# Kernel tuning notes

Hardware: AMD Instinct MI355X
Metric: run time of the kernel (lower is better)

## Reference

```python
import jax, jax.numpy as jnp
import numpy as np

K = 3          # kernel size
STRIDE = 1
PAD = 1        # dilation*(K-1)//2
DIL = 1


def _bilinear_gather(x, py, px):
    """Bilinear sample x[B,C,H,W] at float coords (py,px) of shape [B,K2,Ho,Wo].
    Out-of-bounds contributions are zero (matches detectron2 DeformConv).
    Returns [B,C,K2,Ho,Wo]."""
    B, C, H, W = x.shape
    xf = x.reshape(B, C, H * W)
    y0 = jnp.floor(py)
    x0 = jnp.floor(px)
    out = jnp.zeros((B, C) + py.shape[1:], dtype=x.dtype)
    gather = jax.vmap(lambda xb, ib: xb[:, ib])  # ([C,HW],[K2,Ho,Wo])->[C,K2,Ho,Wo]
    for cy, cx in ((y0, x0), (y0, x0 + 1.0), (y0 + 1.0, x0), (y0 + 1.0, x0 + 1.0)):
        wgt = (1.0 - jnp.abs(py - cy)) * (1.0 - jnp.abs(px - cx))
        valid = (cy >= 0) & (cy <= H - 1) & (cx >= 0) & (cx <= W - 1)
        yi = jnp.clip(cy, 0, H - 1).astype(jnp.int32)
        xi = jnp.clip(cx, 0, W - 1).astype(jnp.int32)
        idx = yi * W + xi  # [B,K2,Ho,Wo]
        vals = gather(xf, idx)  # [B,C,K2,Ho,Wo]
        out = out + (wgt * valid.astype(x.dtype))[:, None] * vals
    return out


def _deform_conv(x, offset, weight):
    B, C, H, W = x.shape
    Ho = (H + 2 * PAD - (DIL * (K - 1) + 1)) // STRIDE + 1
    Wo = (W + 2 * PAD - (DIL * (K - 1) + 1)) // STRIDE + 1
    K2 = K * K
    # base sampling grid
    hs = (jnp.arange(Ho) * STRIDE - PAD).astype(x.dtype)  # [Ho]
    ws = (jnp.arange(Wo) * STRIDE - PAD).astype(x.dtype)  # [Wo]
    ky, kx = jnp.meshgrid(jnp.arange(K), jnp.arange(K), indexing='ij')
    ky = (ky.reshape(-1) * DIL).astype(x.dtype)  # [K2], row-major taps
    kx = (kx.reshape(-1) * DIL).astype(x.dtype)
    # offsets: channel 2k = dy, 2k+1 = dx for tap k
    off = offset.reshape(B, K2, 2, Ho, Wo)
    dy, dx = off[:, :, 0], off[:, :, 1]  # [B,K2,Ho,Wo]
    py = hs[None, None, :, None] + ky[None, :, None, None] + dy
    px = ws[None, None, None, :] + kx[None, :, None, None] + dx
    sampled = _bilinear_gather(x, py, px)  # [B,C,K2,Ho,Wo]
    wk = weight.reshape(weight.shape[0], C, K2)  # groups=1
    return jnp.einsum('ocK,bcKhw->bohw', wk, sampled)


def setup_inputs() -> dict:
    key = jax.random.key(0)
    k1, k2, k3 = jax.random.split(key, 3)
    B, C, H, W = 8, 256, 64, 64
    x = jax.random.normal(k1, (B, C, H, W), dtype=jnp.float32)
    offset = jax.random.normal(k2, (B, 2 * K * K, H, W), dtype=jnp.float32)
    weight = jax.random.normal(k3, (256, C, K, K), dtype=jnp.float32) * 0.02
    return {"x": x, "offset": offset, "weight": weight}


def reference(x, offset, weight):
    return _deform_conv(x, offset, weight)
```

## Files before the change

### kernel.cpp

```cpp
#include <hip/hip_runtime.h>
#include <stdint.h>


#define Bb 8
#define Cc 256
#define Hh 64
#define Ww 64
#define Pp 4096
#define Oo 256
#define NK2 9
#define NPAIR 36
#define BN 64
#define SROW 40
#define WT_BYTES (2u * 72u * 256u * 32u)

typedef __attribute__((ext_vector_type(4))) float f32x4;
typedef __attribute__((ext_vector_type(8))) short s16x8;
typedef __attribute__((ext_vector_type(4))) int   i32x4;

static __device__ __forceinline__ unsigned short f2bf(float f) {
    union { float f; uint32_t u; } v; v.f = f;
    return (unsigned short)((v.u + 0x7fffu + ((v.u >> 16) & 1u)) >> 16);
}
static __device__ __forceinline__ int imin(int a, int b) { return a < b ? a : b; }
static __device__ __forceinline__ int imax(int a, int b) { return a > b ? a : b; }

__global__ __launch_bounds__(256)
void prep(const float* __restrict__ x, const float* __restrict__ w,
          unsigned short* __restrict__ xt, unsigned short* __restrict__ wt) {
    __shared__ __align__(16) unsigned short L[9216];
    const int bx = blockIdx.x, tid = threadIdx.x;

    if (bx < 2048) {
        unsigned short (*t2)[72] = (unsigned short(*)[72])L;
        const int b = bx & 7, ti = bx >> 3;
        const int c0 = (ti & 3) * 64, p0 = (ti >> 2) * 64;
        #pragma unroll
        for (int rd = 0; rd < 4; rd++) {
            int c = (tid >> 4) + rd * 16;
            int px4 = (tid & 15) * 4;
            f32x4 fv = *(const f32x4*)&x[(size_t)(b * Cc + c0 + c) * Pp + p0 + px4];
            #pragma unroll
            for (int j = 0; j < 4; j++) {
                int px = px4 + j;
                int chunk = ((c >> 3) + px) & 7;
                t2[px][chunk * 8 + (c & 7)] = f2bf(fv[j]);
            }
        }
        __syncthreads();
        #pragma unroll
        for (int rd = 0; rd < 2; rd++) {
            int px = (tid >> 3) + rd * 32;
            int k = tid & 7;
            int chunk = (k + px) & 7;
            uint4 u = *(const uint4*)&t2[px][chunk * 8];
            *(uint4*)&xt[(size_t)(b * Pp + p0 + px) * Cc + c0 + k * 8] = u;
        }
    } else {
        const int o0 = (bx - 2048) * 4;
        #pragma unroll
        for (int r9 = 0; r9 < 9; r9++) {
            int idx = r9 * 256 + tid;
            f32x4 fv = *(const f32x4*)&w[(size_t)o0 * 2304 + (size_t)idx * 4];
            #pragma unroll
            for (int j = 0; j < 4; j++) L[idx * 4 + j] = f2bf(fv[j]);
        }
        __syncthreads();
        #pragma unroll 4
        for (int i = 0; i < 36; i++) {
            int ks = i * 2 + (tid >> 7);
            int r = (tid >> 5) & 3, c32 = tid & 31;
            int c = (ks & 7) * 32 + c32, k2 = ks >> 3;
            wt[(size_t)ks * 8192 + (o0 + r) * 32 + c32] = L[r * 2304 + c * 9 + k2];
        }
    }
}

__global__ __launch_bounds__(512, 4)
void dcn_main(const float* __restrict__ off, const unsigned short* __restrict__ wt,
              const unsigned short* __restrict__ xt, float* __restrict__ out) {
    __shared__ __align__(16) unsigned short Sl[2][2][BN][SROW];
    __shared__ __align__(16) int   tidx[NK2][BN][4];
    __shared__ __align__(16) float twgt[NK2][BN][4];

    const int b   = blockIdx.x & 7;
    const int p0  = (blockIdx.x >> 3) * BN;
    const int tid = threadIdx.x;
    const int lane = tid & 63;
    const int wv   = tid >> 6;
    const int quad = lane >> 4;
    const int l16  = lane & 15;
    const int moff = wv * 32;

    const int px  = tid >> 3;
    const int sub = tid & 7;
    const int hh_ = sub >> 2;
    const int cc_ = (sub & 3) * 8;

    const char* xtb = (const char*)xt + (size_t)b * Pp * Cc * 2;

    for (int t = tid; t < NK2 * BN; t += 512) {
        int k2 = t >> 6, pxl = t & 63;
        int pl = p0 + pxl;
        int hh = pl >> 6, ww = pl & 63;
        int ky = k2 / 3, kx = k2 - ky * 3;
        float dy = off[((size_t)(b * 18 + 2 * k2    ) * Pp) + pl];
        float dx = off[((size_t)(b * 18 + 2 * k2 + 1) * Pp) + pl];
        float py  = (float)(hh - 1 + ky) + dy;
        float pxf = (float)(ww - 1 + kx) + dx;
        float y0f = floorf(py), x0f = floorf(pxf);
        int   y0 = (int)y0f,  x0 = (int)x0f;
        int   y1 = y0 + 1,    x1 = x0 + 1;
        float ly = py - y0f,  lx = pxf - x0f;
        float oy = 1.f - ly,  ox = 1.f - lx;
        bool vy0 = (y0 >= 0) && (y0 < Hh);
        bool vy1 = (y1 >= 0) && (y1 < Hh);
        bool vx0 = (x0 >= 0) && (x0 < Ww);
        bool vx1 = (x1 >= 0) && (x1 < Ww);
        int cy0 = imin(imax(y0, 0), Hh - 1), cy1 = imin(imax(y1, 0), Hh - 1);
        int cx0 = imin(imax(x0, 0), Ww - 1), cx1 = imin(imax(x1, 0), Ww - 1);
        tidx[k2][pxl][0] = (cy0 * Ww + cx0) * 512;  twgt[k2][pxl][0] = (vy0 && vx0) ? oy * ox : 0.f;
        tidx[k2][pxl][1] = (cy0 * Ww + cx1) * 512;  twgt[k2][pxl][1] = (vy0 && vx1) ? oy * lx : 0.f;
        tidx[k2][pxl][2] = (cy1 * Ww + cx0) * 512;  twgt[k2][pxl][2] = (vy1 && vx0) ? ly * ox : 0.f;
        tidx[k2][pxl][3] = (cy1 * Ww + cx1) * 512;  twgt[k2][pxl][3] = (vy1 && vx1) ? ly * lx : 0.f;
    }
    __syncthreads();

    int   tio[4];
    float twv[4];
    uint4 g[4];
    {
        i32x4 ti = *(const i32x4*)&tidx[0][px][0];
        f32x4 tw = *(const f32x4*)&twgt[0][px][0];
        #pragma unroll
        for (int t = 0; t < 4; t++) { tio[t] = ti[t]; twv[t] = tw[t]; }
    }

    f32x4 acc[2][4];
    #pragma unroll
    for (int mt = 0; mt < 2; mt++)
        #pragma unroll
        for (int nt = 0; nt < 4; nt++) acc[mt][nt] = (f32x4){0.f, 0.f, 0.f, 0.f};

    auto reduce_store = [&](int prn) {
        float s0 = 0.f, s1 = 0.f, s2 = 0.f, s3 = 0.f, s4 = 0.f, s5 = 0.f, s6 = 0.f, s7 = 0.f;
        #pragma unroll
        for (int t = 0; t < 4; t++) {
            uint4 v = g[t];
            float wg = twv[t];
            s0 += wg * __uint_as_float(v.x << 16);
            s1 += wg * __uint_as_float(v.x);
            s2 += wg * __uint_as_float(v.y << 16);
            s3 += wg * __uint_as_float(v.y);
            s4 += wg * __uint_as_float(v.z << 16);
            s5 += wg * __uint_as_float(v.z);
            s6 += wg * __uint_as_float(v.w << 16);
            s7 += wg * __uint_as_float(v.w);
        }
        uint4 d;
        d.x = __builtin_amdgcn_perm(__float_as_uint(s1), __float_as_uint(s0), 0x07060302u);
        d.y = __builtin_amdgcn_perm(__float_as_uint(s3), __float_as_uint(s2), 0x07060302u);
        d.z = __builtin_amdgcn_perm(__float_as_uint(s5), __float_as_uint(s4), 0x07060302u);
        d.w = __builtin_amdgcn_perm(__float_as_uint(s7), __float_as_uint(s6), 0x07060302u);
        *(uint4*)&Sl[prn & 1][hh_][px][cc_] = d;
    };

    s16x8 afA[2][2], afB[2][2];

    auto step = [&](int pr, s16x8 (&cur)[2][2], s16x8 (&nxt)[2][2]) {
        __syncthreads();
        const int prn = pr + 1;
        if (prn < NPAIR) {
            if ((prn & 3) == 0) {
                int k2 = prn >> 2;
                i32x4 ti = *(const i32x4*)&tidx[k2][px][0];
                f32x4 tw = *(const f32x4*)&twgt[k2][px][0];
                #pragma unroll
                for (int t = 0; t < 4; t++) { tio[t] = ti[t]; twv[t] = tw[t]; }
            }
            const int coff = (prn & 3) * 128 + sub * 16;
            #pragma unroll
            for (int t = 0; t < 4; t++)
                g[t] = *(const uint4*)(xtb + tio[t] + coff);
            const char* wb = (const char*)wt + ((size_t)prn << 15);
            #pragma unroll
            for (int h = 0; h < 2; h++)
                #pragma unroll
                for (int mt = 0; mt < 2; mt++)
                    nxt[h][mt] = *(const s16x8*)(wb + h * 16384 +
                                                 (moff + mt * 16 + l16) * 64 + quad * 16);
        }
        s16x8 bfr[2][4];
        const char* sb = (const char*)&Sl[pr & 1][0][0][0];
        #pragma unroll
        for (int h = 0; h < 2; h++)
            #pragma unroll
            for (int nt = 0; nt < 4; nt++)
                bfr[h][nt] = *(const s16x8*)(sb + h * (BN * SROW * 2) +
                                             (nt * 16 + l16) * (SROW * 2) + quad * 16);
        #pragma unroll
        for (int h = 0; h < 2; h++)
            #pragma unroll
            for (int mt = 0; mt < 2; mt++)
                #pragma unroll
                for (int nt = 0; nt < 4; nt++)
                    acc[mt][nt] = __builtin_amdgcn_mfma_f32_16x16x32_bf16(
                        cur[h][mt], bfr[h][nt], acc[mt][nt], 0, 0, 0);
        if (prn < NPAIR) reduce_store(prn);
    };

    {
        #pragma unroll
        for (int t = 0; t < 4; t++)
            g[t] = *(const uint4*)(xtb + tio[t] + sub * 16);
        const char* wb = (const char*)wt;
        #pragma unroll
        for (int h = 0; h < 2; h++)
            #pragma unroll
            for (int mt = 0; mt < 2; mt++)
                afA[h][mt] = *(const s16x8*)(wb + h * 16384 +
                                             (moff + mt * 16 + l16) * 64 + quad * 16);
        reduce_store(0);
    }

    for (int pr = 0; pr < NPAIR; pr += 2) {
        step(pr,     afA, afB);
        step(pr + 1, afB, afA);
    }

    float* op = out + ((size_t)b * Oo) * Pp + p0;
    #pragma unroll
    for (int mt = 0; mt < 2; mt++)
        #pragma unroll
        for (int nt = 0; nt < 4; nt++)
            #pragma unroll
            for (int r = 0; r < 4; r++) {
                int o_ = moff + mt * 16 + quad * 4 + r;
                int p_ = nt * 16 + l16;
                op[(size_t)o_ * Pp + p_] = acc[mt][nt][r];
            }
}

extern "C" void kernel_launch(void* const* d_in, const int* in_sizes, int n_in,
                              void* d_out, int out_size, void* d_ws, size_t ws_size,
                              hipStream_t stream) {
    (void)in_sizes; (void)n_in; (void)out_size; (void)ws_size;
    const float* x   = (const float*)d_in[0];
    const float* off = (const float*)d_in[1];
    const float* w   = (const float*)d_in[2];
    float* out = (float*)d_out;

    unsigned short* wt = (unsigned short*)d_ws;
    unsigned short* xt = (unsigned short*)((char*)d_ws + WT_BYTES);

    hipLaunchKernelGGL(prep, dim3(2112), dim3(256), 0, stream, x, w, xt, wt);
    hipLaunchKernelGGL(dcn_main, dim3(512), dim3(512), 0, stream, off, wt, xt, out);
}
```

Baseline: 147.5 us.

## Halve pixel tile to 32 with 256-thread blocks and simplify software pipeline

The main kernel now processes 32 pixels per block with 4 waves, each computing 64 output channels, and launches twice as many blocks. The register double-buffered weight fragments and deferred gather are replaced by a simpler loop that loads weights and samples the next slice inline before the MFMAs. The prep kernel's LDS swizzle is also changed to rotate by groups of 8 pixels. The aim is more blocks and occupancy with less register pressure, at the cost of re-reading weights across more blocks and exposing global load latency that was previously hidden.

```diff
diff --git a/kernel.cpp b/kernel.cpp
--- a/kernel.cpp
+++ b/kernel.cpp
@@ -10,7 +10,7 @@
 #define Oo 256
 #define NK2 9
 #define NPAIR 36
-#define BN 64
+#define BN 32
 #define SROW 40
 #define WT_BYTES (2u * 72u * 256u * 32u)
 
@@ -43,7 +43,7 @@
             #pragma unroll
             for (int j = 0; j < 4; j++) {
                 int px = px4 + j;
-                int chunk = ((c >> 3) + px) & 7;
+                int chunk = ((c >> 3) + (px >> 3)) & 7;
                 t2[px][chunk * 8 + (c & 7)] = f2bf(fv[j]);
             }
         }
@@ -52,7 +52,7 @@
         for (int rd = 0; rd < 2; rd++) {
             int px = (tid >> 3) + rd * 32;
             int k = tid & 7;
-            int chunk = (k + px) & 7;
+            int chunk = (k + (px >> 3)) & 7;
             uint4 u = *(const uint4*)&t2[px][chunk * 8];
             *(uint4*)&xt[(size_t)(b * Pp + p0 + px) * Cc + c0 + k * 8] = u;
         }
@@ -76,7 +76,7 @@
     }
 }
 
-__global__ __launch_bounds__(512, 4)
+__global__ __launch_bounds__(256, 4)
 void dcn_main(const float* __restrict__ off, const unsigned short* __restrict__ wt,
               const unsigned short* __restrict__ xt, float* __restrict__ out) {
     __shared__ __align__(16) unsigned short Sl[2][2][BN][SROW];
@@ -90,7 +90,7 @@
     const int wv   = tid >> 6;
     const int quad = lane >> 4;
     const int l16  = lane & 15;
-    const int moff = wv * 32;
+    const int moff = wv * 64;
 
     const int px  = tid >> 3;
     const int sub = tid & 7;
@@ -99,8 +99,8 @@
 
     const char* xtb = (const char*)xt + (size_t)b * Pp * Cc * 2;
 
-    for (int t = tid; t < NK2 * BN; t += 512) {
-        int k2 = t >> 6, pxl = t & 63;
+    for (int t = tid; t < NK2 * BN; t += 256) {
+        int k2 = t >> 5, pxl = t & 31;
         int pl = p0 + pxl;
         int hh = pl >> 6, ww = pl & 63;
         int ky = k2 / 3, kx = k2 - ky * 3;
@@ -128,7 +128,6 @@
 
     int   tio[4];
     float twv[4];
-    uint4 g[4];
     {
         i32x4 ti = *(const i32x4*)&tidx[0][px][0];
         f32x4 tw = *(const f32x4*)&twgt[0][px][0];
@@ -136,17 +135,12 @@
         for (int t = 0; t < 4; t++) { tio[t] = ti[t]; twv[t] = tw[t]; }
     }
 
-    f32x4 acc[2][4];
-    #pragma unroll
-    for (int mt = 0; mt < 2; mt++)
-        #pragma unroll
-        for (int nt = 0; nt < 4; nt++) acc[mt][nt] = (f32x4){0.f, 0.f, 0.f, 0.f};
-
-    auto reduce_store = [&](int prn) {
+    auto sample_into = [&](int pr) {
+        int coff = (pr & 3) * 128 + sub * 16;
         float s0 = 0.f, s1 = 0.f, s2 = 0.f, s3 = 0.f, s4 = 0.f, s5 = 0.f, s6 = 0.f, s7 = 0.f;
         #pragma unroll
         for (int t = 0; t < 4; t++) {
-            uint4 v = g[t];
+            uint4 v = *(const uint4*)(xtb + tio[t] + coff);
             float wg = twv[t];
             s0 += wg * __uint_as_float(v.x << 16);
             s1 += wg * __uint_as_float(v.x);
@@ -162,14 +156,30 @@
         d.y = __builtin_amdgcn_perm(__float_as_uint(s3), __float_as_uint(s2), 0x07060302u);
         d.z = __builtin_amdgcn_perm(__float_as_uint(s5), __float_as_uint(s4), 0x07060302u);
         d.w = __builtin_amdgcn_perm(__float_as_uint(s7), __float_as_uint(s6), 0x07060302u);
-        *(uint4*)&Sl[prn & 1][hh_][px][cc_] = d;
+        *(uint4*)&Sl[pr & 1][hh_][px][cc_] = d;
     };
 
-    s16x8 afA[2][2], afB[2][2];
-
-    auto step = [&](int pr, s16x8 (&cur)[2][2], s16x8 (&nxt)[2][2]) {
+    f32x4 acc[4][2];
+    #pragma unroll
+    for (int mt = 0; mt < 4; mt++)
+        #pragma unroll
+        for (int nt = 0; nt < 2; nt++) acc[mt][nt] = (f32x4){0.f, 0.f, 0.f, 0.f};
+
+    sample_into(0);
+
+    for (int pr = 0; pr < NPAIR; pr++) {
         __syncthreads();
-        const int prn = pr + 1;
+
+        const char* wb = (const char*)wt + ((size_t)pr << 15);
+        s16x8 af[2][4];
+        #pragma unroll
+        for (int h = 0; h < 2; h++)
+            #pragma unroll
+            for (int mt = 0; mt < 4; mt++)
+                af[h][mt] = *(const s16x8*)(wb + h * 16384 +
+                                            (moff + mt * 16 + l16) * 64 + quad * 16);
+
+        int prn = pr + 1;
         if (prn < NPAIR) {
             if ((prn & 3) == 0) {
                 int k2 = prn >> 2;
@@ -178,61 +188,29 @@
                 #pragma unroll
                 for (int t = 0; t < 4; t++) { tio[t] = ti[t]; twv[t] = tw[t]; }
             }
-            const int coff = (prn & 3) * 128 + sub * 16;
-            #pragma unroll
-            for (int t = 0; t < 4; t++)
-                g[t] = *(const uint4*)(xtb + tio[t] + coff);
-            const char* wb = (const char*)wt + ((size_t)prn << 15);
-            #pragma unroll
-            for (int h = 0; h < 2; h++)
+            sample_into(prn);
+        }
+
+        #pragma unroll
+        for (int h = 0; h < 2; h++) {
+            s16x8 bfr[2];
+            #pragma unroll
+            for (int nt = 0; nt < 2; nt++)
+                bfr[nt] = *(const s16x8*)&Sl[pr & 1][h][nt * 16 + l16][quad * 8];
+            #pragma unroll
+            for (int mt = 0; mt < 4; mt++)
                 #pragma unroll
-                for (int mt = 0; mt < 2; mt++)
-                    nxt[h][mt] = *(const s16x8*)(wb + h * 16384 +
-                                                 (moff + mt * 16 + l16) * 64 + quad * 16);
-        }
-        s16x8 bfr[2][4];
-        const char* sb = (const char*)&Sl[pr & 1][0][0][0];
-        #pragma unroll
-        for (int h = 0; h < 2; h++)
-            #pragma unroll
-            for (int nt = 0; nt < 4; nt++)
-                bfr[h][nt] = *(const s16x8*)(sb + h * (BN * SROW * 2) +
-                                             (nt * 16 + l16) * (SROW * 2) + quad * 16);
-        #pragma unroll
-        for (int h = 0; h < 2; h++)
-            #pragma unroll
-            for (int mt = 0; mt < 2; mt++)
-                #pragma unroll
-                for (int nt = 0; nt < 4; nt++)
+                for (int nt = 0; nt < 2; nt++)
                     acc[mt][nt] = __builtin_amdgcn_mfma_f32_16x16x32_bf16(
-                        cur[h][mt], bfr[h][nt], acc[mt][nt], 0, 0, 0);
-        if (prn < NPAIR) reduce_store(prn);
-    };
-
-    {
-        #pragma unroll
-        for (int t = 0; t < 4; t++)
-            g[t] = *(const uint4*)(xtb + tio[t] + sub * 16);
-        const char* wb = (const char*)wt;
-        #pragma unroll
-        for (int h = 0; h < 2; h++)
-            #pragma unroll
-            for (int mt = 0; mt < 2; mt++)
-                afA[h][mt] = *(const s16x8*)(wb + h * 16384 +
-                                             (moff + mt * 16 + l16) * 64 + quad * 16);
-        reduce_store(0);
-    }
-
-    for (int pr = 0; pr < NPAIR; pr += 2) {
-        step(pr,     afA, afB);
-        step(pr + 1, afB, afA);
+                        af[h][mt], bfr[nt], acc[mt][nt], 0, 0, 0);
+        }
     }
 
     float* op = out + ((size_t)b * Oo) * Pp + p0;
     #pragma unroll
-    for (int mt = 0; mt < 2; mt++)
-        #pragma unroll
-        for (int nt = 0; nt < 4; nt++)
+    for (int mt = 0; mt < 4; mt++)
+        #pragma unroll
+        for (int nt = 0; nt < 2; nt++)
             #pragma unroll
             for (int r = 0; r < 4; r++) {
                 int o_ = moff + mt * 16 + quad * 4 + r;
@@ -254,5 +232,5 @@
     unsigned short* xt = (unsigned short*)((char*)d_ws + WT_BYTES);
 
     hipLaunchKernelGGL(prep, dim3(2112), dim3(256), 0, stream, x, w, xt, wt);
-    hipLaunchKernelGGL(dcn_main, dim3(512), dim3(512), 0, stream, off, wt, xt, out);
-}
+    hipLaunchKernelGGL(dcn_main, dim3(1024), dim3(256), 0, stream, off, wt, xt, out);
+}
```

Result: slower. 175.5 us (+19.0%).
